# Kernel tuning notes

Hardware: AMD Instinct MI355X
Metric: run time of the kernel (lower is better)

The kernel has to match this reference:

```python
import jax, jax.numpy as jnp
import numpy as np

B, T, D, H = 2, 2048, 1024, 16
DH = D // H  # 64


def setup_inputs() -> dict:
    key = jax.random.key(0)
    ks = jax.random.split(key, 6)
    s = 1.0 / np.sqrt(D)
    return {
        "x": jax.random.normal(ks[0], (B, T, D), dtype=jnp.float32),
        "Wq": jax.random.normal(ks[1], (D, D), dtype=jnp.float32) * s,
        "Wk": jax.random.normal(ks[2], (D, D), dtype=jnp.float32) * s,
        "Wv": jax.random.normal(ks[3], (D, D), dtype=jnp.float32) * s,
        "Wo": jax.random.normal(ks[4], (D, D), dtype=jnp.float32) * s,
        "bo": jnp.zeros((D,), dtype=jnp.float32),
    }


def reference(x, Wq, Wk, Wv, Wo, bo):
    b, t, _ = x.shape
    # projections (torch Linear: x @ W.T; here W stored as [d_in, d_out])
    q = (x @ Wq).reshape(b, t, H, DH).transpose(0, 2, 1, 3)  # [b,H,t,dh]
    k = (x @ Wk).reshape(b, t, H, DH).transpose(0, 2, 1, 3)
    v = (x @ Wv).reshape(b, t, H, DH).transpose(0, 2, 1, 3)
    scores = jnp.einsum("bhqd,bhkd->bhqk", q, k) / np.sqrt(DH).astype(np.float32)
    causal = jnp.tril(jnp.ones((t, t), dtype=bool))  # True = keep
    scores = jnp.where(causal, scores, -jnp.inf)
    weights = jax.nn.softmax(scores, axis=-1)
    ctx = jnp.einsum("bhqk,bhkd->bhqd", weights, v)
    ctx = ctx.transpose(0, 2, 1, 3).reshape(b, t, D)
    return ctx @ Wo + bo
```

## Files before the change

### kernel.cpp

```cpp
#include <hip/hip_runtime.h>


typedef unsigned short u16;
typedef __attribute__((ext_vector_type(8))) short short8;
typedef __attribute__((ext_vector_type(4))) float f32x4;

#define B_ 2
#define T_ 2048
#define D_ 1024
#define H_ 16
#define DH_ 64
#define M_ (B_ * T_)
#define SCALE_LOG2E 0.18033688011112042f
#define NEG_BIG -3.0e4f

#define GLOAD16(g, l)                                                     \
  __builtin_amdgcn_global_load_lds(                                       \
      (const __attribute__((address_space(1))) void*)(g),                 \
      (__attribute__((address_space(3))) void*)(l), 16, 0, 0)

__device__ __forceinline__ u16 f2bf(float f) {
  union { float f; unsigned u; } v; v.f = f;
  unsigned r = v.u + 0x7fffu + ((v.u >> 16) & 1u);
  return (u16)(r >> 16);
}
__device__ __forceinline__ u16 f2bf_trunc(float f) {
  union { float f; unsigned u; } v; v.f = f;
  return (u16)(v.u >> 16);
}

__global__ __launch_bounds__(256) void cvt_x(const float* __restrict__ x,
                                             u16* __restrict__ xb) {
  const int i = (blockIdx.x * 256 + threadIdx.x) * 8;
  float4 a = *(const float4*)(x + i);
  float4 b = *(const float4*)(x + i + 4);
  short8 o;
  o[0] = (short)f2bf(a.x); o[1] = (short)f2bf(a.y);
  o[2] = (short)f2bf(a.z); o[3] = (short)f2bf(a.w);
  o[4] = (short)f2bf(b.x); o[5] = (short)f2bf(b.y);
  o[6] = (short)f2bf(b.z); o[7] = (short)f2bf(b.w);
  *(short8*)(xb + i) = o;
}

__global__ __launch_bounds__(256) void transpose_w(
    const float* __restrict__ w0, const float* __restrict__ w1,
    const float* __restrict__ w2, const float* __restrict__ w3,
    u16* __restrict__ outT) {
  __shared__ u16 Tl[64][72];
  const int z = blockIdx.z;
  const float* src = (z == 0) ? w0 : (z == 1) ? w1 : (z == 2) ? w2 : w3;
  const int r0 = blockIdx.y * 64, c0 = blockIdx.x * 64;
  const int tid = threadIdx.x;
  const int rr = tid >> 2, cc = (tid & 3) * 16;

  const float* p = src + (size_t)(r0 + rr) * D_ + c0 + cc;
  float4 f0 = *(const float4*)p;
  float4 f1 = *(const float4*)(p + 4);
  float4 f2 = *(const float4*)(p + 8);
  float4 f3 = *(const float4*)(p + 12);
  Tl[rr][cc + 0] = f2bf(f0.x); Tl[rr][cc + 1] = f2bf(f0.y);
  Tl[rr][cc + 2] = f2bf(f0.z); Tl[rr][cc + 3] = f2bf(f0.w);
  Tl[rr][cc + 4] = f2bf(f1.x); Tl[rr][cc + 5] = f2bf(f1.y);
  Tl[rr][cc + 6] = f2bf(f1.z); Tl[rr][cc + 7] = f2bf(f1.w);
  Tl[rr][cc + 8] = f2bf(f2.x); Tl[rr][cc + 9] = f2bf(f2.y);
  Tl[rr][cc +10] = f2bf(f2.z); Tl[rr][cc +11] = f2bf(f2.w);
  Tl[rr][cc +12] = f2bf(f3.x); Tl[rr][cc +13] = f2bf(f3.y);
  Tl[rr][cc +14] = f2bf(f3.z); Tl[rr][cc +15] = f2bf(f3.w);
  __syncthreads();

  u16* o = outT + (size_t)z * D_ * D_ + (size_t)(c0 + rr) * D_ + r0 + cc;
  short8 x0, x1;
#pragma unroll
  for (int i = 0; i < 8; i++) x0[i] = (short)Tl[cc + i][rr];
#pragma unroll
  for (int i = 0; i < 8; i++) x1[i] = (short)Tl[cc + 8 + i][rr];
  *(short8*)o = x0;
  *(short8*)(o + 8) = x1;
}

__global__ __launch_bounds__(256) void qkv_gemm(
    const u16* __restrict__ x, const u16* __restrict__ wT,
    u16* __restrict__ qkv) {
  __shared__ u16 As[128][32];
  __shared__ u16 Bs[128][32];

  const int z = blockIdx.z;
  const u16* W = wT + (size_t)z * D_ * D_;
  u16* out = qkv + (size_t)z * M_ * D_;
  const int n0 = blockIdx.x * 128;
  const int m0 = blockIdx.y * 128;
  const int tid = threadIdx.x;
  const int lane = tid & 63, w = tid >> 6;
  const int quad = lane >> 4, l16 = lane & 15;
  const int wr = w >> 1, wc = w & 1;

  f32x4 acc[4][4] = {};
  const int grow = w * 16 + (lane >> 2);
  const int gcol = (lane & 3) * 8;
  u16* lA = (u16*)As + w * 512;
  u16* lB = (u16*)Bs + w * 512;

  for (int k0 = 0; k0 < D_; k0 += 32) {
    const u16* gA = x + (size_t)(m0 + grow) * D_ + k0 + gcol;
    const u16* gB = W + (size_t)(n0 + grow) * D_ + k0 + gcol;
    GLOAD16(gA, lA);
    GLOAD16(gA + (size_t)64 * D_, lA + 2048);
    GLOAD16(gB, lB);
    GLOAD16(gB + (size_t)64 * D_, lB + 2048);
    __syncthreads();

    short8 af[4], bf[4];
#pragma unroll
    for (int i = 0; i < 4; i++)
      af[i] = *(const short8*)&As[wr * 64 + i * 16 + l16][quad * 8];
#pragma unroll
    for (int i = 0; i < 4; i++)
      bf[i] = *(const short8*)&Bs[wc * 64 + i * 16 + l16][quad * 8];
#pragma unroll
    for (int i = 0; i < 4; i++)
#pragma unroll
      for (int j = 0; j < 4; j++)
        acc[i][j] = __builtin_amdgcn_mfma_f32_16x16x32_bf16(af[i], bf[j], acc[i][j], 0, 0, 0);
    __syncthreads();
  }

#pragma unroll
  for (int i = 0; i < 4; i++) {
#pragma unroll
    for (int j = 0; j < 4; j++) {
      const int n = n0 + wc * 64 + j * 16 + l16;
      const int h = n >> 6, dh = n & 63;
#pragma unroll
      for (int r = 0; r < 4; r++) {
        const int m = m0 + wr * 64 + i * 16 + quad * 4 + r;
        const int b = m >> 11, t = m & (T_ - 1);
        out[(((size_t)(b * H_ + h)) * T_ + t) * DH_ + dh] = f2bf(acc[i][j][r]);
      }
    }
  }
}

__global__ __launch_bounds__(256) void transpose_v(
    const u16* __restrict__ v, u16* __restrict__ vT) {
  __shared__ u16 Tl[64][72];
  const int t0 = blockIdx.x * 64;
  const int bh = blockIdx.y;
  const int tid = threadIdx.x;
  const int rr = tid >> 2, cc = (tid & 3) * 16;

  const u16* p = v + (size_t)bh * T_ * DH_ + (size_t)(t0 + rr) * DH_ + cc;
  short8 a0 = *(const short8*)p;
  short8 a1 = *(const short8*)(p + 8);
  *(short8*)&Tl[rr][cc] = a0;
  *(short8*)&Tl[rr][cc + 8] = a1;
  __syncthreads();

  u16* o = vT + (size_t)bh * DH_ * T_ + (size_t)rr * T_ + t0 + cc;
  short8 x0, x1;
#pragma unroll
  for (int i = 0; i < 8; i++) x0[i] = (short)Tl[cc + i][rr];
#pragma unroll
  for (int i = 0; i < 8; i++) x1[i] = (short)Tl[cc + 8 + i][rr];
  *(short8*)o = x0;
  *(short8*)(o + 8) = x1;
}

__global__ __launch_bounds__(128) void attn(
    const u16* __restrict__ qg, const u16* __restrict__ kg,
    const u16* __restrict__ vtg, u16* __restrict__ ctx) {
  __shared__ u16 Ks[64][72];
  __shared__ u16 Vs[64][72];
  __shared__ u16 Ps[2][16][72];

  const int qt = gridDim.x - 1 - blockIdx.x;
  const int bh = blockIdx.y;
  const int tid = threadIdx.x;
  const int w = tid >> 6, lane = tid & 63;
  const int quad = lane >> 4, l16 = lane & 15;
  const int q0 = qt * 32;
  const size_t baseQK = (size_t)bh * T_ * DH_;
  const size_t baseV  = (size_t)bh * DH_ * T_;

  const int qrow = q0 + w * 16 + l16;
  short8 qf0 = *(const short8*)(qg + baseQK + (size_t)qrow * DH_ + quad * 8);
  short8 qf1 = *(const short8*)(qg + baseQK + (size_t)qrow * DH_ + 32 + quad * 8);

  f32x4 oacc[4] = {};
  float mi = NEG_BIG, li = 0.f;

  const int srow = tid >> 1;
  const int scol = (tid & 1) * 32;
  const int kvend = q0 + 32;

  {
    const u16* kp = kg + baseQK + (size_t)srow * DH_ + scol;
    const u16* vp = vtg + baseV + (size_t)srow * T_ + scol;
    short8 kr0 = *(const short8*)kp;
    short8 kr1 = *(const short8*)(kp + 8);
    short8 kr2 = *(const short8*)(kp + 16);
    short8 kr3 = *(const short8*)(kp + 24);
    short8 vr0 = *(const short8*)vp;
    short8 vr1 = *(const short8*)(vp + 8);
    short8 vr2 = *(const short8*)(vp + 16);
    short8 vr3 = *(const short8*)(vp + 24);

    for (int kv0 = 0; kv0 < kvend; kv0 += 64) {
      __syncthreads();
      *(short8*)&Ks[srow][scol]      = kr0;
      *(short8*)&Ks[srow][scol + 8]  = kr1;
      *(short8*)&Ks[srow][scol + 16] = kr2;
      *(short8*)&Ks[srow][scol + 24] = kr3;
      *(short8*)&Vs[srow][scol]      = vr0;
      *(short8*)&Vs[srow][scol + 8]  = vr1;
      *(short8*)&Vs[srow][scol + 16] = vr2;
      *(short8*)&Vs[srow][scol + 24] = vr3;
      if (kv0 + 64 < kvend) {
        const u16* kn = kg + baseQK + (size_t)(kv0 + 64 + srow) * DH_ + scol;
        const u16* vn = vtg + baseV + (size_t)srow * T_ + kv0 + 64 + scol;
        kr0 = *(const short8*)kn;
        kr1 = *(const short8*)(kn + 8);
        kr2 = *(const short8*)(kn + 16);
        kr3 = *(const short8*)(kn + 24);
        vr0 = *(const short8*)vn;
        vr1 = *(const short8*)(vn + 8);
        vr2 = *(const short8*)(vn + 16);
        vr3 = *(const short8*)(vn + 24);
      }
      __syncthreads();

      float s[4][4];
#pragma unroll
      for (int cb = 0; cb < 4; cb++) {
        f32x4 sv = {};
        short8 kf0 = *(const short8*)&Ks[cb * 16 + l16][quad * 8];
        short8 kf1 = *(const short8*)&Ks[cb * 16 + l16][32 + quad * 8];
        sv = __builtin_amdgcn_mfma_f32_16x16x32_bf16(kf0, qf0, sv, 0, 0, 0);
        sv = __builtin_amdgcn_mfma_f32_16x16x32_bf16(kf1, qf1, sv, 0, 0, 0);
#pragma unroll
        for (int r = 0; r < 4; r++) {
          const int kv = kv0 + cb * 16 + quad * 4 + r;
          s[cb][r] = (kv <= qrow) ? sv[r] * SCALE_LOG2E : NEG_BIG;
        }
      }

      float mloc = NEG_BIG;
#pragma unroll
      for (int cb = 0; cb < 4; cb++)
#pragma unroll
        for (int r = 0; r < 4; r++) mloc = fmaxf(mloc, s[cb][r]);
      mloc = fmaxf(mloc, __shfl_xor(mloc, 16, 64));
      mloc = fmaxf(mloc, __shfl_xor(mloc, 32, 64));
      const float mnew = fmaxf(mi, mloc);
      const float alpha = exp2f(mi - mnew);
      mi = mnew;
      float rs = 0.f;
      float p[4][4];
#pragma unroll
      for (int cb = 0; cb < 4; cb++)
#pragma unroll
        for (int r = 0; r < 4; r++) { p[cb][r] = exp2f(s[cb][r] - mnew); rs += p[cb][r]; }
      rs += __shfl_xor(rs, 16, 64);
      rs += __shfl_xor(rs, 32, 64);
      li = li * alpha + rs;
#pragma unroll
      for (int cb = 0; cb < 4; cb++)
#pragma unroll
        for (int r = 0; r < 4; r++) oacc[cb][r] *= alpha;

#pragma unroll
      for (int cb = 0; cb < 4; cb++)
#pragma unroll
        for (int r = 0; r < 4; r++)
          Ps[w][l16][cb * 16 + quad * 4 + r] = f2bf_trunc(p[cb][r]);

      short8 pa0 = *(const short8*)&Ps[w][l16][quad * 8];
      short8 pa1 = *(const short8*)&Ps[w][l16][32 + quad * 8];
#pragma unroll
      for (int cb = 0; cb < 4; cb++) {
        short8 vf0 = *(const short8*)&Vs[cb * 16 + l16][quad * 8];
        short8 vf1 = *(const short8*)&Vs[cb * 16 + l16][32 + quad * 8];
        oacc[cb] = __builtin_amdgcn_mfma_f32_16x16x32_bf16(vf0, pa0, oacc[cb], 0, 0, 0);
        oacc[cb] = __builtin_amdgcn_mfma_f32_16x16x32_bf16(vf1, pa1, oacc[cb], 0, 0, 0);
      }
    }
  }

  const int b = bh >> 4, h = bh & 15;
  const float inv = 1.0f / li;
#pragma unroll
  for (int cb = 0; cb < 4; cb++) {
#pragma unroll
    for (int r = 0; r < 4; r++) {
      const int dh = cb * 16 + quad * 4 + r;
      ctx[((size_t)(b * T_ + qrow)) * D_ + h * 64 + dh] = f2bf(oacc[cb][r] * inv);
    }
  }
}

__global__ __launch_bounds__(256) void out_gemm(
    const u16* __restrict__ ctx, const u16* __restrict__ woT,
    const float* __restrict__ bo, float* __restrict__ out) {
  __shared__ u16 As[128][32];
  __shared__ u16 Bs[128][32];

  const int n0 = blockIdx.x * 128;
  const int m0 = blockIdx.y * 128;
  const int tid = threadIdx.x;
  const int lane = tid & 63, w = tid >> 6;
  const int quad = lane >> 4, l16 = lane & 15;
  const int wr = w >> 1, wc = w & 1;

  f32x4 acc[4][4] = {};
  const int grow = w * 16 + (lane >> 2);
  const int gcol = (lane & 3) * 8;
  u16* lA = (u16*)As + w * 512;
  u16* lB = (u16*)Bs + w * 512;

  for (int k0 = 0; k0 < D_; k0 += 32) {
    const u16* gA = ctx + (size_t)(m0 + grow) * D_ + k0 + gcol;
    const u16* gB = woT + (size_t)(n0 + grow) * D_ + k0 + gcol;
    GLOAD16(gA, lA);
    GLOAD16(gA + (size_t)64 * D_, lA + 2048);
    GLOAD16(gB, lB);
    GLOAD16(gB + (size_t)64 * D_, lB + 2048);
    __syncthreads();

    short8 af[4], bf[4];
#pragma unroll
    for (int i = 0; i < 4; i++)
      af[i] = *(const short8*)&As[wr * 64 + i * 16 + l16][quad * 8];
#pragma unroll
    for (int i = 0; i < 4; i++)
      bf[i] = *(const short8*)&Bs[wc * 64 + i * 16 + l16][quad * 8];
#pragma unroll
    for (int i = 0; i < 4; i++)
#pragma unroll
      for (int j = 0; j < 4; j++)
        acc[i][j] = __builtin_amdgcn_mfma_f32_16x16x32_bf16(af[i], bf[j], acc[i][j], 0, 0, 0);
    __syncthreads();
  }

#pragma unroll
  for (int i = 0; i < 4; i++) {
#pragma unroll
    for (int j = 0; j < 4; j++) {
      const int n = n0 + wc * 64 + j * 16 + l16;
      const float bias = bo[n];
#pragma unroll
      for (int r = 0; r < 4; r++) {
        const int m = m0 + wr * 64 + i * 16 + quad * 4 + r;
        out[(size_t)m * D_ + n] = acc[i][j][r] + bias;
      }
    }
  }
}

extern "C" void kernel_launch(void* const* d_in, const int* in_sizes, int n_in,
                              void* d_out, int out_size, void* d_ws, size_t ws_size,
                              hipStream_t stream) {
  const float* x  = (const float*)d_in[0];
  const float* Wq = (const float*)d_in[1];
  const float* Wk = (const float*)d_in[2];
  const float* Wv = (const float*)d_in[3];
  const float* Wo = (const float*)d_in[4];
  const float* bo = (const float*)d_in[5];
  float* out = (float*)d_out;

  u16* ws  = (u16*)d_ws;
  u16* xb  = ws;
  u16* wT  = xb + (size_t)M_ * D_;
  u16* qkv = wT + (size_t)4 * D_ * D_;
  u16* ctx = qkv + (size_t)3 * M_ * D_;
  u16* vT  = xb;

  cvt_x<<<dim3(M_ * D_ / (256 * 8)), 256, 0, stream>>>(x, xb);
  transpose_w<<<dim3(16, 16, 4), 256, 0, stream>>>(Wq, Wk, Wv, Wo, wT);
  qkv_gemm<<<dim3(D_ / 128, M_ / 128, 3), 256, 0, stream>>>(xb, wT, qkv);
  transpose_v<<<dim3(T_ / 64, B_ * H_), 256, 0, stream>>>(qkv + (size_t)2 * M_ * D_, vT);
  attn<<<dim3(T_ / 32, B_ * H_), 128, 0, stream>>>(
      qkv, qkv + (size_t)M_ * D_, vT, ctx);
  out_gemm<<<dim3(D_ / 128, M_ / 128), 256, 0, stream>>>(ctx, wT + (size_t)3 * D_ * D_, bo, out);
}
```

Before: 232.8 us.

## Process 64 query rows per attention block and fold softmax scale into Q

```diff
diff --git a/kernel.cpp b/kernel.cpp
--- a/kernel.cpp
+++ b/kernel.cpp
@@ -3,6 +3,7 @@
 
 typedef unsigned short u16;
 typedef __attribute__((ext_vector_type(8))) short short8;
+typedef __attribute__((ext_vector_type(4))) short short4_t;
 typedef __attribute__((ext_vector_type(4))) float f32x4;
 
 #define B_ 2
@@ -124,6 +125,7 @@
     __syncthreads();
   }
 
+  const float osc = (z == 0) ? SCALE_LOG2E : 1.0f;
 #pragma unroll
   for (int i = 0; i < 4; i++) {
 #pragma unroll
@@ -134,7 +136,7 @@
       for (int r = 0; r < 4; r++) {
         const int m = m0 + wr * 64 + i * 16 + quad * 4 + r;
         const int b = m >> 11, t = m & (T_ - 1);
-        out[(((size_t)(b * H_ + h)) * T_ + t) * DH_ + dh] = f2bf(acc[i][j][r]);
+        out[(((size_t)(b * H_ + h)) * T_ + t) * DH_ + dh] = f2bf(acc[i][j][r] * osc);
       }
     }
   }
@@ -170,130 +172,174 @@
     const u16* __restrict__ vtg, u16* __restrict__ ctx) {
   __shared__ u16 Ks[64][72];
   __shared__ u16 Vs[64][72];
-  __shared__ u16 Ps[2][16][72];
+  __shared__ u16 Ps[2][2][16][72];
 
   const int qt = gridDim.x - 1 - blockIdx.x;
   const int bh = blockIdx.y;
   const int tid = threadIdx.x;
   const int w = tid >> 6, lane = tid & 63;
   const int quad = lane >> 4, l16 = lane & 15;
-  const int q0 = qt * 32;
+  const int q0 = qt * 64;
   const size_t baseQK = (size_t)bh * T_ * DH_;
   const size_t baseV  = (size_t)bh * DH_ * T_;
 
-  const int qrow = q0 + w * 16 + l16;
-  short8 qf0 = *(const short8*)(qg + baseQK + (size_t)qrow * DH_ + quad * 8);
-  short8 qf1 = *(const short8*)(qg + baseQK + (size_t)qrow * DH_ + 32 + quad * 8);
-
-  f32x4 oacc[4] = {};
-  float mi = NEG_BIG, li = 0.f;
+  const int qrowA = q0 + w * 32 + l16;
+  const int qrowB = qrowA + 16;
+  short8 qfA0 = *(const short8*)(qg + baseQK + (size_t)qrowA * DH_ + quad * 8);
+  short8 qfA1 = *(const short8*)(qg + baseQK + (size_t)qrowA * DH_ + 32 + quad * 8);
+  short8 qfB0 = *(const short8*)(qg + baseQK + (size_t)qrowB * DH_ + quad * 8);
+  short8 qfB1 = *(const short8*)(qg + baseQK + (size_t)qrowB * DH_ + 32 + quad * 8);
+
+  f32x4 oaccA[4] = {}, oaccB[4] = {};
+  float miA = NEG_BIG, liA = 0.f;
+  float miB = NEG_BIG, liB = 0.f;
 
   const int srow = tid >> 1;
   const int scol = (tid & 1) * 32;
-  const int kvend = q0 + 32;
-
-  {
-    const u16* kp = kg + baseQK + (size_t)srow * DH_ + scol;
-    const u16* vp = vtg + baseV + (size_t)srow * T_ + scol;
-    short8 kr0 = *(const short8*)kp;
-    short8 kr1 = *(const short8*)(kp + 8);
-    short8 kr2 = *(const short8*)(kp + 16);
-    short8 kr3 = *(const short8*)(kp + 24);
-    short8 vr0 = *(const short8*)vp;
-    short8 vr1 = *(const short8*)(vp + 8);
-    short8 vr2 = *(const short8*)(vp + 16);
-    short8 vr3 = *(const short8*)(vp + 24);
-
-    for (int kv0 = 0; kv0 < kvend; kv0 += 64) {
-      __syncthreads();
-      *(short8*)&Ks[srow][scol]      = kr0;
-      *(short8*)&Ks[srow][scol + 8]  = kr1;
-      *(short8*)&Ks[srow][scol + 16] = kr2;
-      *(short8*)&Ks[srow][scol + 24] = kr3;
-      *(short8*)&Vs[srow][scol]      = vr0;
-      *(short8*)&Vs[srow][scol + 8]  = vr1;
-      *(short8*)&Vs[srow][scol + 16] = vr2;
-      *(short8*)&Vs[srow][scol + 24] = vr3;
-      if (kv0 + 64 < kvend) {
-        const u16* kn = kg + baseQK + (size_t)(kv0 + 64 + srow) * DH_ + scol;
-        const u16* vn = vtg + baseV + (size_t)srow * T_ + kv0 + 64 + scol;
-        kr0 = *(const short8*)kn;
-        kr1 = *(const short8*)(kn + 8);
-        kr2 = *(const short8*)(kn + 16);
-        kr3 = *(const short8*)(kn + 24);
-        vr0 = *(const short8*)vn;
-        vr1 = *(const short8*)(vn + 8);
-        vr2 = *(const short8*)(vn + 16);
-        vr3 = *(const short8*)(vn + 24);
-      }
-      __syncthreads();
-
-      float s[4][4];
-#pragma unroll
-      for (int cb = 0; cb < 4; cb++) {
-        f32x4 sv = {};
-        short8 kf0 = *(const short8*)&Ks[cb * 16 + l16][quad * 8];
-        short8 kf1 = *(const short8*)&Ks[cb * 16 + l16][32 + quad * 8];
-        sv = __builtin_amdgcn_mfma_f32_16x16x32_bf16(kf0, qf0, sv, 0, 0, 0);
-        sv = __builtin_amdgcn_mfma_f32_16x16x32_bf16(kf1, qf1, sv, 0, 0, 0);
+
+  const u16* kp = kg + baseQK + (size_t)srow * DH_ + scol;
+  const u16* vp = vtg + baseV + (size_t)srow * T_ + scol;
+  short8 kr0 = *(const short8*)kp;
+  short8 kr1 = *(const short8*)(kp + 8);
+  short8 kr2 = *(const short8*)(kp + 16);
+  short8 kr3 = *(const short8*)(kp + 24);
+  short8 vr0 = *(const short8*)vp;
+  short8 vr1 = *(const short8*)(vp + 8);
+  short8 vr2 = *(const short8*)(vp + 16);
+  short8 vr3 = *(const short8*)(vp + 24);
+
+  for (int kv0 = 0; kv0 <= q0; kv0 += 64) {
+    __syncthreads();
+    *(short8*)&Ks[srow][scol]      = kr0;
+    *(short8*)&Ks[srow][scol + 8]  = kr1;
+    *(short8*)&Ks[srow][scol + 16] = kr2;
+    *(short8*)&Ks[srow][scol + 24] = kr3;
+    *(short8*)&Vs[srow][scol]      = vr0;
+    *(short8*)&Vs[srow][scol + 8]  = vr1;
+    *(short8*)&Vs[srow][scol + 16] = vr2;
+    *(short8*)&Vs[srow][scol + 24] = vr3;
+    if (kv0 < q0) {
+      const u16* kn = kg + baseQK + (size_t)(kv0 + 64 + srow) * DH_ + scol;
+      const u16* vn = vtg + baseV + (size_t)srow * T_ + kv0 + 64 + scol;
+      kr0 = *(const short8*)kn;
+      kr1 = *(const short8*)(kn + 8);
+      kr2 = *(const short8*)(kn + 16);
+      kr3 = *(const short8*)(kn + 24);
+      vr0 = *(const short8*)vn;
+      vr1 = *(const short8*)(vn + 8);
+      vr2 = *(const short8*)(vn + 16);
+      vr3 = *(const short8*)(vn + 24);
+    }
+    __syncthreads();
+
+    short8 kf0[4], kf1[4];
+#pragma unroll
+    for (int cb = 0; cb < 4; cb++) {
+      kf0[cb] = *(const short8*)&Ks[cb * 16 + l16][quad * 8];
+      kf1[cb] = *(const short8*)&Ks[cb * 16 + l16][32 + quad * 8];
+    }
+
+    f32x4 svA[4], svB[4];
+#pragma unroll
+    for (int cb = 0; cb < 4; cb++) {
+      f32x4 z = {};
+      svA[cb] = __builtin_amdgcn_mfma_f32_16x16x32_bf16(kf0[cb], qfA0, z, 0, 0, 0);
+      svA[cb] = __builtin_amdgcn_mfma_f32_16x16x32_bf16(kf1[cb], qfA1, svA[cb], 0, 0, 0);
+      svB[cb] = __builtin_amdgcn_mfma_f32_16x16x32_bf16(kf0[cb], qfB0, z, 0, 0, 0);
+      svB[cb] = __builtin_amdgcn_mfma_f32_16x16x32_bf16(kf1[cb], qfB1, svB[cb], 0, 0, 0);
+    }
+
+    float sA[4][4], sB[4][4];
+    if (kv0 == q0) {
+#pragma unroll
+      for (int cb = 0; cb < 4; cb++)
 #pragma unroll
         for (int r = 0; r < 4; r++) {
           const int kv = kv0 + cb * 16 + quad * 4 + r;
-          s[cb][r] = (kv <= qrow) ? sv[r] * SCALE_LOG2E : NEG_BIG;
+          sA[cb][r] = (kv <= qrowA) ? svA[cb][r] : NEG_BIG;
+          sB[cb][r] = (kv <= qrowB) ? svB[cb][r] : NEG_BIG;
         }
+    } else {
+#pragma unroll
+      for (int cb = 0; cb < 4; cb++)
+#pragma unroll
+        for (int r = 0; r < 4; r++) { sA[cb][r] = svA[cb][r]; sB[cb][r] = svB[cb][r]; }
+    }
+
+    float mlA = NEG_BIG, mlB = NEG_BIG;
+#pragma unroll
+    for (int cb = 0; cb < 4; cb++)
+#pragma unroll
+      for (int r = 0; r < 4; r++) { mlA = fmaxf(mlA, sA[cb][r]); mlB = fmaxf(mlB, sB[cb][r]); }
+    mlA = fmaxf(mlA, __shfl_xor(mlA, 16, 64));
+    mlA = fmaxf(mlA, __shfl_xor(mlA, 32, 64));
+    mlB = fmaxf(mlB, __shfl_xor(mlB, 16, 64));
+    mlB = fmaxf(mlB, __shfl_xor(mlB, 32, 64));
+    const float mnA = fmaxf(miA, mlA), mnB = fmaxf(miB, mlB);
+    const float alA = exp2f(miA - mnA), alB = exp2f(miB - mnB);
+    miA = mnA; miB = mnB;
+    float rsA = 0.f, rsB = 0.f;
+    float pA[4][4], pB[4][4];
+#pragma unroll
+    for (int cb = 0; cb < 4; cb++)
+#pragma unroll
+      for (int r = 0; r < 4; r++) {
+        pA[cb][r] = exp2f(sA[cb][r] - mnA); rsA += pA[cb][r];
+        pB[cb][r] = exp2f(sB[cb][r] - mnB); rsB += pB[cb][r];
       }
-
-      float mloc = NEG_BIG;
-#pragma unroll
-      for (int cb = 0; cb < 4; cb++)
-#pragma unroll
-        for (int r = 0; r < 4; r++) mloc = fmaxf(mloc, s[cb][r]);
-      mloc = fmaxf(mloc, __shfl_xor(mloc, 16, 64));
-      mloc = fmaxf(mloc, __shfl_xor(mloc, 32, 64));
-      const float mnew = fmaxf(mi, mloc);
-      const float alpha = exp2f(mi - mnew);
-      mi = mnew;
-      float rs = 0.f;
-      float p[4][4];
-#pragma unroll
-      for (int cb = 0; cb < 4; cb++)
-#pragma unroll
-        for (int r = 0; r < 4; r++) { p[cb][r] = exp2f(s[cb][r] - mnew); rs += p[cb][r]; }
-      rs += __shfl_xor(rs, 16, 64);
-      rs += __shfl_xor(rs, 32, 64);
-      li = li * alpha + rs;
-#pragma unroll
-      for (int cb = 0; cb < 4; cb++)
-#pragma unroll
-        for (int r = 0; r < 4; r++) oacc[cb][r] *= alpha;
-
-#pragma unroll
-      for (int cb = 0; cb < 4; cb++)
-#pragma unroll
-        for (int r = 0; r < 4; r++)
-          Ps[w][l16][cb * 16 + quad * 4 + r] = f2bf_trunc(p[cb][r]);
-
-      short8 pa0 = *(const short8*)&Ps[w][l16][quad * 8];
-      short8 pa1 = *(const short8*)&Ps[w][l16][32 + quad * 8];
-#pragma unroll
-      for (int cb = 0; cb < 4; cb++) {
-        short8 vf0 = *(const short8*)&Vs[cb * 16 + l16][quad * 8];
-        short8 vf1 = *(const short8*)&Vs[cb * 16 + l16][32 + quad * 8];
-        oacc[cb] = __builtin_amdgcn_mfma_f32_16x16x32_bf16(vf0, pa0, oacc[cb], 0, 0, 0);
-        oacc[cb] = __builtin_amdgcn_mfma_f32_16x16x32_bf16(vf1, pa1, oacc[cb], 0, 0, 0);
+    rsA += __shfl_xor(rsA, 16, 64); rsA += __shfl_xor(rsA, 32, 64);
+    rsB += __shfl_xor(rsB, 16, 64); rsB += __shfl_xor(rsB, 32, 64);
+    liA = liA * alA + rsA; liB = liB * alB + rsB;
+#pragma unroll
+    for (int cb = 0; cb < 4; cb++)
+#pragma unroll
+      for (int r = 0; r < 4; r++) { oaccA[cb][r] *= alA; oaccB[cb][r] *= alB; }
+
+    short8 vf0[4], vf1[4];
+#pragma unroll
+    for (int cb = 0; cb < 4; cb++) {
+      vf0[cb] = *(const short8*)&Vs[cb * 16 + l16][quad * 8];
+      vf1[cb] = *(const short8*)&Vs[cb * 16 + l16][32 + quad * 8];
+    }
+
+#pragma unroll
+    for (int cb = 0; cb < 4; cb++) {
+      short4_t pkA, pkB;
+#pragma unroll
+      for (int r = 0; r < 4; r++) {
+        pkA[r] = (short)f2bf_trunc(pA[cb][r]);
+        pkB[r] = (short)f2bf_trunc(pB[cb][r]);
       }
+      *(short4_t*)&Ps[w][0][l16][cb * 16 + quad * 4] = pkA;
+      *(short4_t*)&Ps[w][1][l16][cb * 16 + quad * 4] = pkB;
+    }
+    short8 paA0 = *(const short8*)&Ps[w][0][l16][quad * 8];
+    short8 paA1 = *(const short8*)&Ps[w][0][l16][32 + quad * 8];
+    short8 paB0 = *(const short8*)&Ps[w][1][l16][quad * 8];
+    short8 paB1 = *(const short8*)&Ps[w][1][l16][32 + quad * 8];
+#pragma unroll
+    for (int cb = 0; cb < 4; cb++) {
+      oaccA[cb] = __builtin_amdgcn_mfma_f32_16x16x32_bf16(vf0[cb], paA0, oaccA[cb], 0, 0, 0);
+      oaccA[cb] = __builtin_amdgcn_mfma_f32_16x16x32_bf16(vf1[cb], paA1, oaccA[cb], 0, 0, 0);
+      oaccB[cb] = __builtin_amdgcn_mfma_f32_16x16x32_bf16(vf0[cb], paB0, oaccB[cb], 0, 0, 0);
+      oaccB[cb] = __builtin_amdgcn_mfma_f32_16x16x32_bf16(vf1[cb], paB1, oaccB[cb], 0, 0, 0);
     }
   }
 
   const int b = bh >> 4, h = bh & 15;
-  const float inv = 1.0f / li;
+  const float invA = 1.0f / liA, invB = 1.0f / liB;
+  u16* outA = ctx + ((size_t)(b * T_ + qrowA)) * D_ + h * 64 + quad * 4;
+  u16* outB = ctx + ((size_t)(b * T_ + qrowB)) * D_ + h * 64 + quad * 4;
 #pragma unroll
   for (int cb = 0; cb < 4; cb++) {
+    short4_t oA, oB;
 #pragma unroll
     for (int r = 0; r < 4; r++) {
-      const int dh = cb * 16 + quad * 4 + r;
-      ctx[((size_t)(b * T_ + qrow)) * D_ + h * 64 + dh] = f2bf(oacc[cb][r] * inv);
-    }
+      oA[r] = (short)f2bf(oaccA[cb][r] * invA);
+      oB[r] = (short)f2bf(oaccB[cb][r] * invB);
+    }
+    *(short4_t*)(outA + cb * 16) = oA;
+    *(short4_t*)(outB + cb * 16) = oB;
   }
 }
 
@@ -377,7 +423,7 @@
   transpose_w<<<dim3(16, 16, 4), 256, 0, stream>>>(Wq, Wk, Wv, Wo, wT);
   qkv_gemm<<<dim3(D_ / 128, M_ / 128, 3), 256, 0, stream>>>(xb, wT, qkv);
   transpose_v<<<dim3(T_ / 64, B_ * H_), 256, 0, stream>>>(qkv + (size_t)2 * M_ * D_, vT);
-  attn<<<dim3(T_ / 32, B_ * H_), 128, 0, stream>>>(
+  attn<<<dim3(T_ / 64, B_ * H_), 128, 0, stream>>>(
       qkv, qkv + (size_t)M_ * D_, vT, ctx);
   out_gemm<<<dim3(D_ / 128, M_ / 128), 256, 0, stream>>>(ctx, wT + (size_t)3 * D_ * D_, bo, out);
 }
```

Measured after the change: 231.0 us. Within noise of the previous version (-0.8%).
